# Kernel tuning notes

Measured on AMD Instinct MI355X. Metric: run time of the kernel, lower is better.

The kernel has to match this reference:

```python
import jax, jax.numpy as jnp
import numpy as np

NUM_EXPERTS = 8
HIDDEN = 1024
FFN = 2048
TOKENS = 2048


def setup_inputs() -> dict:
    key = jax.random.key(0)
    k_x, k_idx, k_w1, k_w2 = jax.random.split(key, 4)
    scale = 0.02
    x = jax.random.normal(k_x, (TOKENS, HIDDEN), dtype=jnp.float32)
    expert_indices = jax.random.randint(k_idx, (TOKENS,), 0, NUM_EXPERTS, dtype=jnp.int64)
    W1 = jax.random.normal(k_w1, (NUM_EXPERTS, HIDDEN, FFN), dtype=jnp.float32) * scale
    b1 = jnp.zeros((NUM_EXPERTS, FFN), dtype=jnp.float32)
    W2 = jax.random.normal(k_w2, (NUM_EXPERTS, FFN, HIDDEN), dtype=jnp.float32) * scale
    b2 = jnp.zeros((NUM_EXPERTS, HIDDEN), dtype=jnp.float32)
    return {"x": x, "expert_indices": expert_indices, "W1": W1, "b1": b1, "W2": W2, "b2": b2}


def reference(x, expert_indices, W1, b1, W2, b2):
    # Each token routed to one expert's MLP: Linear -> GELU(exact) -> Linear.
    # Dropout is identity in eval mode. Loop is over the small fixed expert set.
    out = jnp.zeros_like(x)
    for e in range(NUM_EXPERTS):
        h = jax.nn.gelu(x @ W1[e] + b1[e], approximate=False)  # [T, FFN]
        y = h @ W2[e] + b2[e]                                   # [T, H]
        mask = (expert_indices == e)[:, None]
        out = out + jnp.where(mask, y, 0.0)
    return out
```

## Files before the change

kernel.cpp:

```cpp
#include <hip/hip_runtime.h>

#define T_TOK 2048
#define HID   1024
#define FFN   2048
#define NEXP  8
#define MAX_SLOTS 40

typedef __attribute__((ext_vector_type(8))) short bf16x8;
typedef __attribute__((ext_vector_type(4))) float f32x4;

__device__ __forceinline__ short f2bf(float f) {
    unsigned u = __builtin_bit_cast(unsigned, f);
    u = (u + 0x7fffu + ((u >> 16) & 1u)) >> 16;
    return (short)u;
}

__device__ __forceinline__ float gelu_exact(float x) {
    return 0.5f * x * (1.0f + erff(x * 0.70710678118654752f));
}

__device__ __forceinline__ int swz(int row, int k) {
    return row * 64 + ((((k >> 3) + row) & 7) << 3) + (k & 7);
}

__global__ void bucket_kernel(const int* __restrict__ idx,
                              int* __restrict__ offs, int* __restrict__ cnts,
                              int* __restrict__ tokl,
                              int* __restrict__ slot_e, int* __restrict__ slot_t0) {
    __shared__ int c[NEXP], cur[NEXP], o[NEXP];
    int tid = threadIdx.x;
    if (tid < NEXP) { c[tid] = 0; cur[tid] = 0; }
    __syncthreads();
    for (int t = tid; t < T_TOK; t += 256) atomicAdd(&c[idx[t]], 1);
    __syncthreads();
    if (tid == 0) {
        int s = 0;
        for (int e = 0; e < NEXP; e++) { o[e] = s; s += c[e]; }
        int ns = 0;
        for (int e = 0; e < NEXP; e++)
            for (int t0 = 0; t0 < c[e]; t0 += 64) {
                slot_e[ns] = e; slot_t0[ns] = t0; ns++;
            }
        for (; ns < MAX_SLOTS; ns++) slot_e[ns] = -1;
    }
    __syncthreads();
    if (tid < NEXP) { offs[tid] = o[tid]; cnts[tid] = c[tid]; }
    for (int t = tid; t < T_TOK; t += 256) {
        int e = idx[t];
        int p = o[e] + atomicAdd(&cur[e], 1);
        tokl[p] = t;
    }
}

__global__ __launch_bounds__(256) void xcvt_kernel(const float* __restrict__ x,
                                                   short* __restrict__ xb) {
    int i = (blockIdx.x * 256 + threadIdx.x) * 8;
    float4 v0 = *(const float4*)(x + i);
    float4 v1 = *(const float4*)(x + i + 4);
    bf16x8 r = {f2bf(v0.x), f2bf(v0.y), f2bf(v0.z), f2bf(v0.w),
                f2bf(v1.x), f2bf(v1.y), f2bf(v1.z), f2bf(v1.w)};
    *(bf16x8*)(xb + i) = r;
}

__global__ __launch_bounds__(256) void initout_kernel(const int* __restrict__ idx,
                                                      const float* __restrict__ b2,
                                                      float* __restrict__ out) {
    int t = blockIdx.x;
    int e = idx[t];
    const float4* src = (const float4*)(b2 + (size_t)e * HID);
    float4* dst = (float4*)(out + (size_t)t * HID);
    dst[threadIdx.x] = src[threadIdx.x];
}

__global__ __launch_bounds__(256) void gemm1_kernel(
        const short* __restrict__ xb, const float* __restrict__ W1,
        const float* __restrict__ b1,
        const int* __restrict__ offs, const int* __restrict__ cnts,
        const int* __restrict__ tokl,
        const int* __restrict__ slot_e, const int* __restrict__ slot_t0,
        short* __restrict__ hg) {
    int s = blockIdx.y;
    int e = slot_e[s];
    if (e < 0) return;
    int t0 = slot_t0[s];
    int count = cnts[e];
    int off = offs[e];
    int n0 = blockIdx.x * 64;

    __shared__ short As[2][64 * 64];
    __shared__ short Bs[2][64 * 64];
    __shared__ int stok[64];

    int tid = threadIdx.x;
    if (tid < 64) {
        int p = t0 + tid;
        stok[tid] = tokl[off + (p < count ? p : count - 1)];
    }
    __syncthreads();

    const float* Bsrc = W1 + (size_t)e * HID * FFN + n0;

    int w = tid >> 6, lane = tid & 63, l15 = lane & 15, quad = lane >> 4;
    int wm = (w >> 1) * 32, wn = (w & 1) * 32;
    int ar = tid >> 3, ac = (tid & 7) * 8;
    int bn = tid & 63, bw = tid >> 6;

    f32x4 acc[2][2];
#pragma unroll
    for (int i = 0; i < 2; i++)
#pragma unroll
        for (int j = 0; j < 2; j++) acc[i][j] = (f32x4){0.f, 0.f, 0.f, 0.f};

    bf16x8 pA0, pA1;
    float pB[16];

#define G1_LOADA(K0) { \
    pA0 = *(const bf16x8*)(xb + (size_t)stok[ar] * HID + (K0) + ac); \
    pA1 = *(const bf16x8*)(xb + (size_t)stok[ar + 32] * HID + (K0) + ac); }
#define G1_LOADB(K0) { \
    _Pragma("unroll") for (int i = 0; i < 4; i++) \
    _Pragma("unroll") for (int j = 0; j < 4; j++) \
        pB[i * 4 + j] = Bsrc[(size_t)((K0) + bw * 16 + i * 4 + j) * FFN + bn]; }
#define G1_STORE(BUF) { \
    *(bf16x8*)&As[BUF][swz(ar, ac)] = pA0; \
    *(bf16x8*)&As[BUF][swz(ar + 32, ac)] = pA1; \
    _Pragma("unroll") for (int i = 0; i < 4; i++) { \
        short4 sv = make_short4(f2bf(pB[i*4]), f2bf(pB[i*4+1]), f2bf(pB[i*4+2]), f2bf(pB[i*4+3])); \
        *(short4*)&Bs[BUF][swz(bn, bw * 16 + i * 4)] = sv; } }

    G1_LOADA(0); G1_LOADB(0);
    G1_STORE(0);

    for (int kt = 0; kt < 16; kt++) {
        __syncthreads();
        int cur = kt & 1;
        if (kt < 15) { G1_LOADA((kt + 1) * 64); G1_LOADB((kt + 1) * 64); }
#pragma unroll
        for (int kk = 0; kk < 2; kk++) {
            int kc = kk * 32 + quad * 8;
            bf16x8 a0 = *(const bf16x8*)&As[cur][swz(wm + l15, kc)];
            bf16x8 a1 = *(const bf16x8*)&As[cur][swz(wm + 16 + l15, kc)];
            bf16x8 b0 = *(const bf16x8*)&Bs[cur][swz(wn + l15, kc)];
            bf16x8 b1v = *(const bf16x8*)&Bs[cur][swz(wn + 16 + l15, kc)];
            acc[0][0] = __builtin_amdgcn_mfma_f32_16x16x32_bf16(a0, b0, acc[0][0], 0, 0, 0);
            acc[0][1] = __builtin_amdgcn_mfma_f32_16x16x32_bf16(a0, b1v, acc[0][1], 0, 0, 0);
            acc[1][0] = __builtin_amdgcn_mfma_f32_16x16x32_bf16(a1, b0, acc[1][0], 0, 0, 0);
            acc[1][1] = __builtin_amdgcn_mfma_f32_16x16x32_bf16(a1, b1v, acc[1][1], 0, 0, 0);
        }
        if (kt < 15) G1_STORE(1 - cur);
    }

#pragma unroll
    for (int mt = 0; mt < 2; mt++) {
        int rbase = wm + mt * 16 + quad * 4;
#pragma unroll
        for (int nt = 0; nt < 2; nt++) {
            int coln = n0 + wn + nt * 16 + l15;
            float bb = b1[e * FFN + coln];
#pragma unroll
            for (int r = 0; r < 4; r++) {
                int p = t0 + rbase + r;
                if (p < count) {
                    float hv = gelu_exact(acc[mt][nt][r] + bb);
                    hg[(size_t)(off + p) * FFN + coln] = f2bf(hv);
                }
            }
        }
    }
}

__global__ __launch_bounds__(256) void gemm2_kernel(
        const short* __restrict__ hg, const float* __restrict__ W2,
        const int* __restrict__ offs, const int* __restrict__ cnts,
        const int* __restrict__ tokl,
        const int* __restrict__ slot_e, const int* __restrict__ slot_t0,
        float* __restrict__ out) {
    int s = blockIdx.y;
    int e = slot_e[s];
    if (e < 0) return;
    int t0 = slot_t0[s];
    int ks = blockIdx.z;
    int count = cnts[e];
    int off = offs[e];
    int n0 = blockIdx.x * 64;
    int kbase = ks * (FFN / 2);

    __shared__ short As[2][64 * 64];
    __shared__ short Bs[2][64 * 64];

    int tid = threadIdx.x;
    const float* Bsrc = W2 + (size_t)e * FFN * HID + n0;

    int w = tid >> 6, lane = tid & 63, l15 = lane & 15, quad = lane >> 4;
    int wm = (w >> 1) * 32, wn = (w & 1) * 32;
    int ar = tid >> 3, ac = (tid & 7) * 8;
    int bn = tid & 63, bw = tid >> 6;

    int ga0 = off + (t0 + ar      < count ? t0 + ar      : count - 1);
    int ga1 = off + (t0 + ar + 32 < count ? t0 + ar + 32 : count - 1);

    f32x4 acc[2][2];
#pragma unroll
    for (int i = 0; i < 2; i++)
#pragma unroll
        for (int j = 0; j < 2; j++) acc[i][j] = (f32x4){0.f, 0.f, 0.f, 0.f};

    bf16x8 pA0, pA1;
    float pB[16];

#define G2_LOADA(K0) { \
    pA0 = *(const bf16x8*)(hg + (size_t)ga0 * FFN + (K0) + ac); \
    pA1 = *(const bf16x8*)(hg + (size_t)ga1 * FFN + (K0) + ac); }
#define G2_LOADB(K0) { \
    _Pragma("unroll") for (int i = 0; i < 4; i++) \
    _Pragma("unroll") for (int j = 0; j < 4; j++) \
        pB[i * 4 + j] = Bsrc[(size_t)((K0) + bw * 16 + i * 4 + j) * HID + bn]; }
#define G2_STORE(BUF) { \
    *(bf16x8*)&As[BUF][swz(ar, ac)] = pA0; \
    *(bf16x8*)&As[BUF][swz(ar + 32, ac)] = pA1; \
    _Pragma("unroll") for (int i = 0; i < 4; i++) { \
        short4 sv = make_short4(f2bf(pB[i*4]), f2bf(pB[i*4+1]), f2bf(pB[i*4+2]), f2bf(pB[i*4+3])); \
        *(short4*)&Bs[BUF][swz(bn, bw * 16 + i * 4)] = sv; } }

    G2_LOADA(kbase); G2_LOADB(kbase);
    G2_STORE(0);

    for (int kt = 0; kt < 16; kt++) {
        __syncthreads();
        int cur = kt & 1;
        if (kt < 15) { G2_LOADA(kbase + (kt + 1) * 64); G2_LOADB(kbase + (kt + 1) * 64); }
#pragma unroll
        for (int kk = 0; kk < 2; kk++) {
            int kc = kk * 32 + quad * 8;
            bf16x8 a0 = *(const bf16x8*)&As[cur][swz(wm + l15, kc)];
            bf16x8 a1 = *(const bf16x8*)&As[cur][swz(wm + 16 + l15, kc)];
            bf16x8 b0 = *(const bf16x8*)&Bs[cur][swz(wn + l15, kc)];
            bf16x8 b1v = *(const bf16x8*)&Bs[cur][swz(wn + 16 + l15, kc)];
            acc[0][0] = __builtin_amdgcn_mfma_f32_16x16x32_bf16(a0, b0, acc[0][0], 0, 0, 0);
            acc[0][1] = __builtin_amdgcn_mfma_f32_16x16x32_bf16(a0, b1v, acc[0][1], 0, 0, 0);
            acc[1][0] = __builtin_amdgcn_mfma_f32_16x16x32_bf16(a1, b0, acc[1][0], 0, 0, 0);
            acc[1][1] = __builtin_amdgcn_mfma_f32_16x16x32_bf16(a1, b1v, acc[1][1], 0, 0, 0);
        }
        if (kt < 15) G2_STORE(1 - cur);
    }

#pragma unroll
    for (int mt = 0; mt < 2; mt++) {
        int rbase = wm + mt * 16 + quad * 4;
#pragma unroll
        for (int nt = 0; nt < 2; nt++) {
            int coln = n0 + wn + nt * 16 + l15;
#pragma unroll
            for (int r = 0; r < 4; r++) {
                int p = t0 + rbase + r;
                if (p < count) {
                    int tok = tokl[off + p];
                    atomicAdd(out + (size_t)tok * HID + coln, acc[mt][nt][r]);
                }
            }
        }
    }
}

extern "C" void kernel_launch(void* const* d_in, const int* in_sizes, int n_in,
                              void* d_out, int out_size, void* d_ws, size_t ws_size,
                              hipStream_t stream) {
    const float* x   = (const float*)d_in[0];
    const int*   idx = (const int*)d_in[1];
    const float* W1  = (const float*)d_in[2];
    const float* b1  = (const float*)d_in[3];
    const float* W2  = (const float*)d_in[4];
    const float* b2  = (const float*)d_in[5];
    float* out = (float*)d_out;

    const size_t META = 32768;
    int*   offs    = (int*)d_ws;
    int*   cnts    = offs + 8;
    int*   tokl    = offs + 16;
    int*   slot_e  = offs + 16 + T_TOK;
    int*   slot_t0 = slot_e + MAX_SLOTS;
    short* xb      = (short*)((char*)d_ws + META);
    short* hg      = (short*)((char*)d_ws + META + (size_t)T_TOK * HID * 2);

    bucket_kernel<<<1, 256, 0, stream>>>(idx, offs, cnts, tokl, slot_e, slot_t0);
    xcvt_kernel<<<T_TOK * HID / (256 * 8), 256, 0, stream>>>(x, xb);
    initout_kernel<<<T_TOK, 256, 0, stream>>>(idx, b2, out);

    gemm1_kernel<<<dim3(FFN / 64, MAX_SLOTS), 256, 0, stream>>>(
        xb, W1, b1, offs, cnts, tokl, slot_e, slot_t0, hg);
    gemm2_kernel<<<dim3(HID / 64, MAX_SLOTS, 2), 256, 0, stream>>>(
        hg, W2, offs, cnts, tokl, slot_e, slot_t0, out);
}
```

Measured before the change: 245.2 us.

## Pre-transpose weights to bf16 and stream GEMM tiles via global_load_lds

Adds a per-call kernel that converts W1 and W2 from fp32 to bf16 and transposes them to N-major, K-contiguous layout. The GEMMs can then fetch both operands as 16-byte chunks directly into LDS with global_load_lds, replacing strided fp32 loads and in-register conversion. The three prep kernels are merged into one launch, and gemm2's split-K goes from 2 to 4. The trade-offs are an extra full pass over the weights each call, and an unpipelined single-buffer K=32 loop with two barriers per step, which exposes load latency.

```diff
diff --git a/kernel.cpp b/kernel.cpp
--- a/kernel.cpp
+++ b/kernel.cpp
@@ -19,61 +19,96 @@
     return 0.5f * x * (1.0f + erff(x * 0.70710678118654752f));
 }
 
-__device__ __forceinline__ int swz(int row, int k) {
-    return row * 64 + ((((k >> 3) + row) & 7) << 3) + (k & 7);
-}
-
-__global__ void bucket_kernel(const int* __restrict__ idx,
-                              int* __restrict__ offs, int* __restrict__ cnts,
-                              int* __restrict__ tokl,
-                              int* __restrict__ slot_e, int* __restrict__ slot_t0) {
-    __shared__ int c[NEXP], cur[NEXP], o[NEXP];
-    int tid = threadIdx.x;
-    if (tid < NEXP) { c[tid] = 0; cur[tid] = 0; }
+__device__ __forceinline__ void async_cp16(const short* g, short* l) {
+    __builtin_amdgcn_global_load_lds(
+        (const __attribute__((address_space(1))) unsigned int*)g,
+        (__attribute__((address_space(3))) unsigned int*)l, 16, 0, 0);
+}
+
+__global__ __launch_bounds__(256) void prep_kernel(
+        const float* __restrict__ x, const int* __restrict__ idx,
+        const float* __restrict__ b2,
+        short* __restrict__ xb, float* __restrict__ out,
+        int* __restrict__ offs, int* __restrict__ cnts,
+        int* __restrict__ tokl,
+        int* __restrict__ slot_e, int* __restrict__ slot_t0) {
+    int bx = blockIdx.x;
+    int tid = threadIdx.x;
+    if (bx < 1024) {
+        int i = (bx * 256 + tid) * 8;
+        float4 v0 = *(const float4*)(x + i);
+        float4 v1 = *(const float4*)(x + i + 4);
+        bf16x8 r = {f2bf(v0.x), f2bf(v0.y), f2bf(v0.z), f2bf(v0.w),
+                    f2bf(v1.x), f2bf(v1.y), f2bf(v1.z), f2bf(v1.w)};
+        *(bf16x8*)(xb + i) = r;
+    } else if (bx < 1024 + T_TOK) {
+        int t = bx - 1024;
+        int e = idx[t];
+        ((float4*)(out + (size_t)t * HID))[tid] =
+            ((const float4*)(b2 + (size_t)e * HID))[tid];
+    } else {
+        __shared__ int c[NEXP], cur[NEXP], o[NEXP];
+        if (tid < NEXP) { c[tid] = 0; cur[tid] = 0; }
+        __syncthreads();
+        for (int t = tid; t < T_TOK; t += 256) atomicAdd(&c[idx[t]], 1);
+        __syncthreads();
+        if (tid == 0) {
+            int s = 0;
+            for (int e = 0; e < NEXP; e++) { o[e] = s; s += c[e]; }
+            int ns = 0;
+            for (int e = 0; e < NEXP; e++)
+                for (int t0 = 0; t0 < c[e]; t0 += 64) {
+                    slot_e[ns] = e; slot_t0[ns] = t0; ns++;
+                }
+            for (; ns < MAX_SLOTS; ns++) slot_e[ns] = -1;
+        }
+        __syncthreads();
+        if (tid < NEXP) { offs[tid] = o[tid]; cnts[tid] = c[tid]; }
+        for (int t = tid; t < T_TOK; t += 256) {
+            int e = idx[t];
+            int p = o[e] + atomicAdd(&cur[e], 1);
+            tokl[p] = t;
+        }
+    }
+}
+
+__global__ __launch_bounds__(256) void wtrans_kernel(
+        const float* __restrict__ W1, const float* __restrict__ W2,
+        short* __restrict__ W1T, short* __restrict__ W2T) {
+    int z = blockIdx.z;
+    const float* W; short* WT; int K, N, e;
+    if (z < NEXP) { W = W1; WT = W1T; K = HID; N = FFN; e = z; }
+    else          { W = W2; WT = W2T; K = FFN; N = HID; e = z - NEXP; }
+    int n0 = blockIdx.x * 64, k0 = blockIdx.y * 64;
+    if (n0 >= N || k0 >= K) return;
+    const float* We = W + (size_t)e * K * N;
+    short* WTe = WT + (size_t)e * N * K;
+    __shared__ short Ts[64][72];
+    int tid = threadIdx.x;
+#pragma unroll
+    for (int i = 0; i < 4; i++) {
+        int c = tid + i * 256;
+        int k = c >> 4, n4 = (c & 15) * 4;
+        float4 v = *(const float4*)(We + (size_t)(k0 + k) * N + n0 + n4);
+        short s0 = f2bf(v.x), s1 = f2bf(v.y), s2 = f2bf(v.z), s3 = f2bf(v.w);
+        int ck = k >> 3, kj = k & 7;
+        Ts[n4 + 0][((ck ^ (((n4 + 0) >> 3) & 7)) << 3) + kj] = s0;
+        Ts[n4 + 1][((ck ^ (((n4 + 1) >> 3) & 7)) << 3) + kj] = s1;
+        Ts[n4 + 2][((ck ^ (((n4 + 2) >> 3) & 7)) << 3) + kj] = s2;
+        Ts[n4 + 3][((ck ^ (((n4 + 3) >> 3) & 7)) << 3) + kj] = s3;
+    }
     __syncthreads();
-    for (int t = tid; t < T_TOK; t += 256) atomicAdd(&c[idx[t]], 1);
-    __syncthreads();
-    if (tid == 0) {
-        int s = 0;
-        for (int e = 0; e < NEXP; e++) { o[e] = s; s += c[e]; }
-        int ns = 0;
-        for (int e = 0; e < NEXP; e++)
-            for (int t0 = 0; t0 < c[e]; t0 += 64) {
-                slot_e[ns] = e; slot_t0[ns] = t0; ns++;
-            }
-        for (; ns < MAX_SLOTS; ns++) slot_e[ns] = -1;
-    }
-    __syncthreads();
-    if (tid < NEXP) { offs[tid] = o[tid]; cnts[tid] = c[tid]; }
-    for (int t = tid; t < T_TOK; t += 256) {
-        int e = idx[t];
-        int p = o[e] + atomicAdd(&cur[e], 1);
-        tokl[p] = t;
-    }
-}
-
-__global__ __launch_bounds__(256) void xcvt_kernel(const float* __restrict__ x,
-                                                   short* __restrict__ xb) {
-    int i = (blockIdx.x * 256 + threadIdx.x) * 8;
-    float4 v0 = *(const float4*)(x + i);
-    float4 v1 = *(const float4*)(x + i + 4);
-    bf16x8 r = {f2bf(v0.x), f2bf(v0.y), f2bf(v0.z), f2bf(v0.w),
-                f2bf(v1.x), f2bf(v1.y), f2bf(v1.z), f2bf(v1.w)};
-    *(bf16x8*)(xb + i) = r;
-}
-
-__global__ __launch_bounds__(256) void initout_kernel(const int* __restrict__ idx,
-                                                      const float* __restrict__ b2,
-                                                      float* __restrict__ out) {
-    int t = blockIdx.x;
-    int e = idx[t];
-    const float4* src = (const float4*)(b2 + (size_t)e * HID);
-    float4* dst = (float4*)(out + (size_t)t * HID);
-    dst[threadIdx.x] = src[threadIdx.x];
+#pragma unroll
+    for (int i = 0; i < 2; i++) {
+        int c = tid + i * 256;
+        int n = c >> 3, ck = c & 7;
+        bf16x8 v = *(const bf16x8*)&Ts[n][(ck ^ ((n >> 3) & 7)) << 3];
+        *(bf16x8*)(WTe + (size_t)(n0 + n) * K + k0 + ck * 8) = v;
+    }
 }
 
 __global__ __launch_bounds__(256) void gemm1_kernel(
-        const short* __restrict__ xb, const float* __restrict__ W1,
+        const short* __restrict__ xb, const short* __restrict__ W1T,
         const float* __restrict__ b1,
         const int* __restrict__ offs, const int* __restrict__ cnts,
         const int* __restrict__ tokl,
@@ -87,8 +122,8 @@
     int off = offs[e];
     int n0 = blockIdx.x * 64;
 
-    __shared__ short As[2][64 * 64];
-    __shared__ short Bs[2][64 * 64];
+    __shared__ short As[64 * 32];
+    __shared__ short Bs[64 * 32];
     __shared__ int stok[64];
 
     int tid = threadIdx.x;
@@ -98,12 +133,15 @@
     }
     __syncthreads();
 
-    const float* Bsrc = W1 + (size_t)e * HID * FFN + n0;
-
     int w = tid >> 6, lane = tid & 63, l15 = lane & 15, quad = lane >> 4;
     int wm = (w >> 1) * 32, wn = (w & 1) * 32;
-    int ar = tid >> 3, ac = (tid & 7) * 8;
-    int bn = tid & 63, bw = tid >> 6;
+
+    int srow = w * 16 + (lane >> 2);
+    int schunk = (lane & 3) * 8;
+    const short* gA = xb + (size_t)stok[srow] * HID + schunk;
+    const short* gB = W1T + (size_t)e * FFN * HID + (size_t)(n0 + srow) * HID + schunk;
+    short* lA = &As[w * 16 * 32];
+    short* lB = &Bs[w * 16 * 32];
 
     f32x4 acc[2][2];
 #pragma unroll
@@ -111,43 +149,19 @@
 #pragma unroll
         for (int j = 0; j < 2; j++) acc[i][j] = (f32x4){0.f, 0.f, 0.f, 0.f};
 
-    bf16x8 pA0, pA1;
-    float pB[16];
-
-#define G1_LOADA(K0) { \
-    pA0 = *(const bf16x8*)(xb + (size_t)stok[ar] * HID + (K0) + ac); \
-    pA1 = *(const bf16x8*)(xb + (size_t)stok[ar + 32] * HID + (K0) + ac); }
-#define G1_LOADB(K0) { \
-    _Pragma("unroll") for (int i = 0; i < 4; i++) \
-    _Pragma("unroll") for (int j = 0; j < 4; j++) \
-        pB[i * 4 + j] = Bsrc[(size_t)((K0) + bw * 16 + i * 4 + j) * FFN + bn]; }
-#define G1_STORE(BUF) { \
-    *(bf16x8*)&As[BUF][swz(ar, ac)] = pA0; \
-    *(bf16x8*)&As[BUF][swz(ar + 32, ac)] = pA1; \
-    _Pragma("unroll") for (int i = 0; i < 4; i++) { \
-        short4 sv = make_short4(f2bf(pB[i*4]), f2bf(pB[i*4+1]), f2bf(pB[i*4+2]), f2bf(pB[i*4+3])); \
-        *(short4*)&Bs[BUF][swz(bn, bw * 16 + i * 4)] = sv; } }
-
-    G1_LOADA(0); G1_LOADB(0);
-    G1_STORE(0);
-
-    for (int kt = 0; kt < 16; kt++) {
-        __syncthreads();
-        int cur = kt & 1;
-        if (kt < 15) { G1_LOADA((kt + 1) * 64); G1_LOADB((kt + 1) * 64); }
-#pragma unroll
-        for (int kk = 0; kk < 2; kk++) {
-            int kc = kk * 32 + quad * 8;
-            bf16x8 a0 = *(const bf16x8*)&As[cur][swz(wm + l15, kc)];
-            bf16x8 a1 = *(const bf16x8*)&As[cur][swz(wm + 16 + l15, kc)];
-            bf16x8 b0 = *(const bf16x8*)&Bs[cur][swz(wn + l15, kc)];
-            bf16x8 b1v = *(const bf16x8*)&Bs[cur][swz(wn + 16 + l15, kc)];
-            acc[0][0] = __builtin_amdgcn_mfma_f32_16x16x32_bf16(a0, b0, acc[0][0], 0, 0, 0);
-            acc[0][1] = __builtin_amdgcn_mfma_f32_16x16x32_bf16(a0, b1v, acc[0][1], 0, 0, 0);
-            acc[1][0] = __builtin_amdgcn_mfma_f32_16x16x32_bf16(a1, b0, acc[1][0], 0, 0, 0);
-            acc[1][1] = __builtin_amdgcn_mfma_f32_16x16x32_bf16(a1, b1v, acc[1][1], 0, 0, 0);
-        }
-        if (kt < 15) G1_STORE(1 - cur);
+    for (int kt = 0; kt < HID / 32; kt++) {
+        async_cp16(gA + kt * 32, lA);
+        async_cp16(gB + kt * 32, lB);
+        __syncthreads();
+        bf16x8 a0 = *(const bf16x8*)&As[(wm + l15) * 32 + quad * 8];
+        bf16x8 a1 = *(const bf16x8*)&As[(wm + 16 + l15) * 32 + quad * 8];
+        bf16x8 b0 = *(const bf16x8*)&Bs[(wn + l15) * 32 + quad * 8];
+        bf16x8 b1v = *(const bf16x8*)&Bs[(wn + 16 + l15) * 32 + quad * 8];
+        acc[0][0] = __builtin_amdgcn_mfma_f32_16x16x32_bf16(a0, b0, acc[0][0], 0, 0, 0);
+        acc[0][1] = __builtin_amdgcn_mfma_f32_16x16x32_bf16(a0, b1v, acc[0][1], 0, 0, 0);
+        acc[1][0] = __builtin_amdgcn_mfma_f32_16x16x32_bf16(a1, b0, acc[1][0], 0, 0, 0);
+        acc[1][1] = __builtin_amdgcn_mfma_f32_16x16x32_bf16(a1, b1v, acc[1][1], 0, 0, 0);
+        __syncthreads();
     }
 
 #pragma unroll
@@ -170,7 +184,7 @@
 }
 
 __global__ __launch_bounds__(256) void gemm2_kernel(
-        const short* __restrict__ hg, const float* __restrict__ W2,
+        const short* __restrict__ hg, const short* __restrict__ W2T,
         const int* __restrict__ offs, const int* __restrict__ cnts,
         const int* __restrict__ tokl,
         const int* __restrict__ slot_e, const int* __restrict__ slot_t0,
@@ -183,21 +197,22 @@
     int count = cnts[e];
     int off = offs[e];
     int n0 = blockIdx.x * 64;
-    int kbase = ks * (FFN / 2);
-
-    __shared__ short As[2][64 * 64];
-    __shared__ short Bs[2][64 * 64];
-
-    int tid = threadIdx.x;
-    const float* Bsrc = W2 + (size_t)e * FFN * HID + n0;
-
+    int kbase = ks * (FFN / 4);
+
+    __shared__ short As[64 * 32];
+    __shared__ short Bs[64 * 32];
+
+    int tid = threadIdx.x;
     int w = tid >> 6, lane = tid & 63, l15 = lane & 15, quad = lane >> 4;
     int wm = (w >> 1) * 32, wn = (w & 1) * 32;
-    int ar = tid >> 3, ac = (tid & 7) * 8;
-    int bn = tid & 63, bw = tid >> 6;
-
-    int ga0 = off + (t0 + ar      < count ? t0 + ar      : count - 1);
-    int ga1 = off + (t0 + ar + 32 < count ? t0 + ar + 32 : count - 1);
+
+    int srow = w * 16 + (lane >> 2);
+    int schunk = (lane & 3) * 8;
+    int grow = off + (t0 + srow < count ? t0 + srow : count - 1);
+    const short* gA = hg + (size_t)grow * FFN + kbase + schunk;
+    const short* gB = W2T + (size_t)e * HID * FFN + (size_t)(n0 + srow) * FFN + kbase + schunk;
+    short* lA = &As[w * 16 * 32];
+    short* lB = &Bs[w * 16 * 32];
 
     f32x4 acc[2][2];
 #pragma unroll
@@ -205,43 +220,19 @@
 #pragma unroll
         for (int j = 0; j < 2; j++) acc[i][j] = (f32x4){0.f, 0.f, 0.f, 0.f};
 
-    bf16x8 pA0, pA1;
-    float pB[16];
-
-#define G2_LOADA(K0) { \
-    pA0 = *(const bf16x8*)(hg + (size_t)ga0 * FFN + (K0) + ac); \
-    pA1 = *(const bf16x8*)(hg + (size_t)ga1 * FFN + (K0) + ac); }
-#define G2_LOADB(K0) { \
-    _Pragma("unroll") for (int i = 0; i < 4; i++) \
-    _Pragma("unroll") for (int j = 0; j < 4; j++) \
-        pB[i * 4 + j] = Bsrc[(size_t)((K0) + bw * 16 + i * 4 + j) * HID + bn]; }
-#define G2_STORE(BUF) { \
-    *(bf16x8*)&As[BUF][swz(ar, ac)] = pA0; \
-    *(bf16x8*)&As[BUF][swz(ar + 32, ac)] = pA1; \
-    _Pragma("unroll") for (int i = 0; i < 4; i++) { \
-        short4 sv = make_short4(f2bf(pB[i*4]), f2bf(pB[i*4+1]), f2bf(pB[i*4+2]), f2bf(pB[i*4+3])); \
-        *(short4*)&Bs[BUF][swz(bn, bw * 16 + i * 4)] = sv; } }
-
-    G2_LOADA(kbase); G2_LOADB(kbase);
-    G2_STORE(0);
-
-    for (int kt = 0; kt < 16; kt++) {
-        __syncthreads();
-        int cur = kt & 1;
-        if (kt < 15) { G2_LOADA(kbase + (kt + 1) * 64); G2_LOADB(kbase + (kt + 1) * 64); }
-#pragma unroll
-        for (int kk = 0; kk < 2; kk++) {
-            int kc = kk * 32 + quad * 8;
-            bf16x8 a0 = *(const bf16x8*)&As[cur][swz(wm + l15, kc)];
-            bf16x8 a1 = *(const bf16x8*)&As[cur][swz(wm + 16 + l15, kc)];
-            bf16x8 b0 = *(const bf16x8*)&Bs[cur][swz(wn + l15, kc)];
-            bf16x8 b1v = *(const bf16x8*)&Bs[cur][swz(wn + 16 + l15, kc)];
-            acc[0][0] = __builtin_amdgcn_mfma_f32_16x16x32_bf16(a0, b0, acc[0][0], 0, 0, 0);
-            acc[0][1] = __builtin_amdgcn_mfma_f32_16x16x32_bf16(a0, b1v, acc[0][1], 0, 0, 0);
-            acc[1][0] = __builtin_amdgcn_mfma_f32_16x16x32_bf16(a1, b0, acc[1][0], 0, 0, 0);
-            acc[1][1] = __builtin_amdgcn_mfma_f32_16x16x32_bf16(a1, b1v, acc[1][1], 0, 0, 0);
-        }
-        if (kt < 15) G2_STORE(1 - cur);
+    for (int kt = 0; kt < FFN / 4 / 32; kt++) {
+        async_cp16(gA + kt * 32, lA);
+        async_cp16(gB + kt * 32, lB);
+        __syncthreads();
+        bf16x8 a0 = *(const bf16x8*)&As[(wm + l15) * 32 + quad * 8];
+        bf16x8 a1 = *(const bf16x8*)&As[(wm + 16 + l15) * 32 + quad * 8];
+        bf16x8 b0 = *(const bf16x8*)&Bs[(wn + l15) * 32 + quad * 8];
+        bf16x8 b1v = *(const bf16x8*)&Bs[(wn + 16 + l15) * 32 + quad * 8];
+        acc[0][0] = __builtin_amdgcn_mfma_f32_16x16x32_bf16(a0, b0, acc[0][0], 0, 0, 0);
+        acc[0][1] = __builtin_amdgcn_mfma_f32_16x16x32_bf16(a0, b1v, acc[0][1], 0, 0, 0);
+        acc[1][0] = __builtin_amdgcn_mfma_f32_16x16x32_bf16(a1, b0, acc[1][0], 0, 0, 0);
+        acc[1][1] = __builtin_amdgcn_mfma_f32_16x16x32_bf16(a1, b1v, acc[1][1], 0, 0, 0);
+        __syncthreads();
     }
 
 #pragma unroll
@@ -279,15 +270,18 @@
     int*   tokl    = offs + 16;
     int*   slot_e  = offs + 16 + T_TOK;
     int*   slot_t0 = slot_e + MAX_SLOTS;
-    short* xb      = (short*)((char*)d_ws + META);
-    short* hg      = (short*)((char*)d_ws + META + (size_t)T_TOK * HID * 2);
-
-    bucket_kernel<<<1, 256, 0, stream>>>(idx, offs, cnts, tokl, slot_e, slot_t0);
-    xcvt_kernel<<<T_TOK * HID / (256 * 8), 256, 0, stream>>>(x, xb);
-    initout_kernel<<<T_TOK, 256, 0, stream>>>(idx, b2, out);
+    char*  base    = (char*)d_ws + META;
+    short* xb  = (short*)base;
+    short* hg  = (short*)(base + (size_t)T_TOK * HID * 2);
+    short* W1T = (short*)(base + (size_t)T_TOK * HID * 2 + (size_t)T_TOK * FFN * 2);
+    short* W2T = W1T + (size_t)NEXP * FFN * HID;
+
+    prep_kernel<<<1024 + T_TOK + 1, 256, 0, stream>>>(
+        x, idx, b2, xb, out, offs, cnts, tokl, slot_e, slot_t0);
+    wtrans_kernel<<<dim3(32, 32, 16), 256, 0, stream>>>(W1, W2, W1T, W2T);
 
     gemm1_kernel<<<dim3(FFN / 64, MAX_SLOTS), 256, 0, stream>>>(
-        xb, W1, b1, offs, cnts, tokl, slot_e, slot_t0, hg);
-    gemm2_kernel<<<dim3(HID / 64, MAX_SLOTS, 2), 256, 0, stream>>>(
-        hg, W2, offs, cnts, tokl, slot_e, slot_t0, out);
-}
+        xb, W1T, b1, offs, cnts, tokl, slot_e, slot_t0, hg);
+    gemm2_kernel<<<dim3(HID / 64, MAX_SLOTS, 4), 256, 0, stream>>>(
+        hg, W2T, offs, cnts, tokl, slot_e, slot_t0, out);
+}
```

Measured after the change: 255.0 us. 4.0% more time.
